# Kernel tuning notes

Measured on AMD Instinct MI355X. Metric: run time of the kernel, lower is better.

The kernel has to match this reference:

```python
import jax, jax.numpy as jnp
import numpy as np

B = 2
D = 256
NH = 8
DH = D // NH
LV = 4
NP_ = 4
NL = 6
DFF = 1024
SHAPES = [(112, 112), (56, 56), (28, 28), (14, 14)]
S = sum(h * w for h, w in SHAPES)


def setup_inputs() -> dict:
    key = jax.random.key(0)
    ks = iter(jax.random.split(key, 64))
    d = {}
    for i, (h, w) in enumerate(SHAPES):
        d[f"src{i}"] = jax.random.normal(next(ks), (B, D, h, w), jnp.float32)
        d[f"pos{i}"] = jax.random.normal(next(ks), (B, D, h, w), jnp.float32)

    def W(*shape, scale=0.02):
        return jax.random.normal(next(ks), shape, jnp.float32) * scale

    d["level_embed"] = W(LV, D, scale=1.0)
    d["off_w"] = W(NL, D, NH * LV * NP_ * 2)
    d["off_b"] = W(NL, NH * LV * NP_ * 2, scale=0.5)
    d["aw_w"] = W(NL, D, NH * LV * NP_)
    d["aw_b"] = jnp.zeros((NL, NH * LV * NP_), jnp.float32)
    d["val_w"] = W(NL, D, D)
    d["val_b"] = jnp.zeros((NL, D), jnp.float32)
    d["out_w"] = W(NL, D, D)
    d["out_b"] = jnp.zeros((NL, D), jnp.float32)
    d["ln1_s"] = jnp.ones((NL, D), jnp.float32)
    d["ln1_b"] = jnp.zeros((NL, D), jnp.float32)
    d["ff1_w"] = W(NL, D, DFF)
    d["ff1_b"] = jnp.zeros((NL, DFF), jnp.float32)
    d["ff2_w"] = W(NL, DFF, D)
    d["ff2_b"] = jnp.zeros((NL, D), jnp.float32)
    d["ln2_s"] = jnp.ones((NL, D), jnp.float32)
    d["ln2_b"] = jnp.zeros((NL, D), jnp.float32)
    return d


def _ln(x, s, b):
    m = jnp.mean(x, -1, keepdims=True)
    v = jnp.mean((x - m) ** 2, -1, keepdims=True)
    return (x - m) / jnp.sqrt(v + 1e-5) * s + b


def _bilinear(v, loc, Hl, Wl):
    # v: [N, DH, Hl, Wl]; loc: [N, Q, P, 2] in [0,1] (grid_sample align_corners=False, zero padding)
    N, Dh = v.shape[0], v.shape[1]
    Q, P = loc.shape[1], loc.shape[2]
    x = loc[..., 0] * Wl - 0.5
    y = loc[..., 1] * Hl - 0.5
    x0f = jnp.floor(x)
    y0f = jnp.floor(y)
    lx = x - x0f
    ly = y - y0f
    x0 = x0f.astype(jnp.int32)
    y0 = y0f.astype(jnp.int32)
    vf = v.reshape(N, Dh, Hl * Wl)

    def g(xi, yi):
        valid = (xi >= 0) & (xi < Wl) & (yi >= 0) & (yi < Hl)
        idx = (jnp.clip(yi, 0, Hl - 1) * Wl + jnp.clip(xi, 0, Wl - 1)).reshape(N, Q * P)
        out = jnp.take_along_axis(vf, idx[:, None, :], axis=2).reshape(N, Dh, Q, P)
        return out * valid[:, None].astype(v.dtype)

    w00 = ((1 - lx) * (1 - ly))[:, None]
    w10 = (lx * (1 - ly))[:, None]
    w01 = ((1 - lx) * ly)[:, None]
    w11 = (lx * ly)[:, None]
    return g(x0, y0) * w00 + g(x0 + 1, y0) * w10 + g(x0, y0 + 1) * w01 + g(x0 + 1, y0 + 1) * w11


def _ms_deform_attn(value, loc, attn):
    # value [B,S,NH,DH], loc [B,S,NH,LV,P,2], attn [B,S,NH,LV,P]
    out = jnp.zeros((B * NH, DH, S), value.dtype)
    s0 = 0
    for l, (Hl, Wl) in enumerate(SHAPES):
        vl = value[:, s0:s0 + Hl * Wl].reshape(B, Hl, Wl, NH, DH)
        vl = vl.transpose(0, 3, 4, 1, 2).reshape(B * NH, DH, Hl, Wl)
        ll = loc[:, :, :, l].transpose(0, 2, 1, 3, 4).reshape(B * NH, S, NP_, 2)
        al = attn[:, :, :, l].transpose(0, 2, 1, 3).reshape(B * NH, S, NP_)[:, None]
        out = out + (_bilinear(vl, ll, Hl, Wl) * al).sum(-1)
        s0 += Hl * Wl
    return out.reshape(B, NH * DH, S).transpose(0, 2, 1)


def _forward(srcs, poss, level_embed, off_w, off_b, aw_w, aw_b, val_w, val_b,
             out_w, out_b, ln1_s, ln1_b, ff1_w, ff1_b, ff2_w, ff2_b, ln2_s, ln2_b):
    src = jnp.concatenate([s.reshape(B, D, -1).transpose(0, 2, 1) for s in srcs], 1)
    pos = jnp.concatenate(
        [p.reshape(B, D, -1).transpose(0, 2, 1) + level_embed[i][None, None] for i, p in enumerate(poss)], 1)
    # reference points: padding masks are all-False => valid_ratios == 1
    refs = []
    for (Hl, Wl) in SHAPES:
        gy, gx = jnp.meshgrid((jnp.arange(Hl) + 0.5) / Hl, (jnp.arange(Wl) + 0.5) / Wl, indexing="ij")
        refs.append(jnp.stack([gx.ravel(), gy.ravel()], -1))
    ref = jnp.concatenate(refs, 0)  # [S, 2]
    normalizer = jnp.array([[w, h] for (h, w) in SHAPES], jnp.float32)  # [LV, 2] = (W, H)
    x = src
    for i in range(NL):
        q = x + pos
        off = (q @ off_w[i] + off_b[i]).reshape(B, S, NH, LV, NP_, 2)
        aw = jax.nn.softmax((q @ aw_w[i] + aw_b[i]).reshape(B, S, NH, LV * NP_), -1)
        aw = aw.reshape(B, S, NH, LV, NP_)
        val = (x @ val_w[i] + val_b[i]).reshape(B, S, NH, DH)
        loc = ref[None, :, None, None, None, :] + off / normalizer[None, None, None, :, None, :]
        attn_out = _ms_deform_attn(val, loc, aw) @ out_w[i] + out_b[i]
        x = _ln(x + attn_out, ln1_s[i], ln1_b[i])
        ff = jax.nn.relu(x @ ff1_w[i] + ff1_b[i]) @ ff2_w[i] + ff2_b[i]
        x = _ln(x + ff, ln2_s[i], ln2_b[i])
    return x


def reference(src0, src1, src2, src3, pos0, pos1, pos2, pos3, level_embed,
              off_w, off_b, aw_w, aw_b, val_w, val_b, out_w, out_b,
              ln1_s, ln1_b, ff1_w, ff1_b, ff2_w, ff2_b, ln2_s, ln2_b):
    memory = _forward([src0, src1, src2, src3], [pos0, pos1, pos2, pos3], level_embed,
                      off_w, off_b, aw_w, aw_b, val_w, val_b, out_w, out_b,
                      ln1_s, ln1_b, ff1_w, ff1_b, ff2_w, ff2_b, ln2_s, ln2_b)
    spatial_shapes = jnp.array(SHAPES, jnp.int32)
    level_start_index = jnp.concatenate(
        [jnp.zeros((1,), jnp.int32), jnp.cumsum(spatial_shapes.prod(1))[:-1].astype(jnp.int32)])
    return memory, spatial_shapes, level_start_index
```

## Files before the change

kernel.cpp:

```cpp
#include <hip/hip_runtime.h>


constexpr int kB  = 2;
constexpr int kD  = 256;
constexpr int kNH = 8;
constexpr int kLV = 4;
constexpr int kNP = 4;
constexpr int kNL = 6;
constexpr int kDFF = 1024;
constexpr int kS  = 16660;
constexpr int kM  = kB * kS;
constexpr int kMp = 33408;
constexpr int kMT64 = kMp / 64;
constexpr int kMT32 = kMp / 32;

typedef short bf16x8 __attribute__((ext_vector_type(8)));
typedef float f32x4  __attribute__((ext_vector_type(4)));

__device__ __forceinline__ unsigned short f2bf(float x) {
  union { float f; unsigned int u; } v; v.f = x;
  unsigned int r = v.u + 0x7FFFu + ((v.u >> 16) & 1u);
  return (unsigned short)(r >> 16);
}
__device__ __forceinline__ float bf2f(unsigned short u) {
  union { unsigned int u; float f; } v; v.u = ((unsigned int)u) << 16;
  return v.f;
}
__device__ __forceinline__ float bflo(unsigned int u) {
  union { unsigned int u; float f; } v; v.u = u << 16;
  return v.f;
}
__device__ __forceinline__ float bfhi(unsigned int u) {
  union { unsigned int u; float f; } v; v.u = u & 0xFFFF0000u;
  return v.f;
}

#define GLOAD_LDS16(gp, lp)                                                    \
  __builtin_amdgcn_global_load_lds(                                            \
      (const __attribute__((address_space(1))) void*)(gp),                     \
      (__attribute__((address_space(3))) void*)(lp), 16, 0, 0)

#define SBARRIER() asm volatile("s_barrier" ::: "memory")

__global__ __launch_bounds__(256) void build_xpos_k(
    const float* __restrict__ src, const float* __restrict__ pos,
    const float* __restrict__ lemb, float* __restrict__ xout,
    float* __restrict__ posout, unsigned short* __restrict__ xbf,
    unsigned short* __restrict__ qbf, int HW, int s0, int lvl)
{
  __shared__ float ts[32][33];
  __shared__ float tp[32][33];
  const int b  = blockIdx.z;
  const int p0 = blockIdx.x * 32, d0 = blockIdx.y * 32;
  const int tx = threadIdx.x, ty = threadIdx.y;
  for (int dd = ty; dd < 32; dd += 8) {
    int p = p0 + tx;
    if (p < HW) {
      size_t idx = ((size_t)b * kD + (d0 + dd)) * (size_t)HW + p;
      ts[dd][tx] = src[idx];
      tp[dd][tx] = pos[idx];
    }
  }
  __syncthreads();
  for (int pp = ty; pp < 32; pp += 8) {
    int p = p0 + pp, d = d0 + tx;
    if (p < HW) {
      size_t o = ((size_t)b * kS + (s0 + p)) * (size_t)kD + d;
      float x = ts[tx][pp];
      float pv = tp[tx][pp] + lemb[lvl * kD + d];
      xout[o] = x;
      posout[o] = pv;
      xbf[o] = f2bf(x);
      qbf[o] = f2bf(x + pv);
    }
  }
}

__global__ __launch_bounds__(256) void wconv_k(
    const float* __restrict__ W, unsigned short* __restrict__ Wt,
    int K, int N, int rowoff, int rowstotal)
{
  __shared__ float t[32][33];
  const int l = blockIdx.z;
  const int n0 = blockIdx.x * 32, k0 = blockIdx.y * 32;
  const int tx = threadIdx.x & 31, ty = threadIdx.x >> 5;
  const float* Wl = W + (size_t)l * K * N;
  unsigned short* Wtl = Wt + (size_t)l * rowstotal * K;
  for (int kk = ty; kk < 32; kk += 8)
    t[kk][tx] = Wl[(size_t)(k0 + kk) * N + n0 + tx];
  __syncthreads();
  for (int nn = ty; nn < 32; nn += 8)
    Wtl[(size_t)(rowoff + n0 + nn) * K + k0 + tx] = f2bf(t[tx][nn]);
}

__global__ __launch_bounds__(256) void biaspack_k(
    const float* __restrict__ ob, const float* __restrict__ ab,
    float* __restrict__ qb)
{
  int i = blockIdx.x * 256 + threadIdx.x;
  if (i >= kNL * 384) return;
  int l = i / 384, c = i - l * 384;
  qb[i] = (c < 256) ? ob[l * 256 + c] : ab[l * 128 + (c - 256)];
}

__global__ __launch_bounds__(256) void refxy_k(float* __restrict__ ref)
{
  int s = blockIdx.x * 256 + threadIdx.x;
  if (s >= kS) return;
  int ls, side;
  if (s < 12544)      { ls = s;         side = 112; }
  else if (s < 15680) { ls = s - 12544; side = 56;  }
  else if (s < 16464) { ls = s - 15680; side = 28;  }
  else                { ls = s - 16464; side = 14;  }
  const float inv = 1.0f / (float)side;
  ref[s * 2 + 0] = ((ls % side) + 0.5f) * inv;
  ref[s * 2 + 1] = ((ls / side) + 0.5f) * inv;
}

template<int RELU, int OUTBF>
__global__ __launch_bounds__(256) void hgemm64_k(
    const unsigned short* __restrict__ A, const unsigned short* __restrict__ Bt,
    const float* __restrict__ bias, void* __restrict__ Cout, int N, int K)
{
  __shared__ unsigned short As[2][64 * 32];
  __shared__ unsigned short Bs[2][128 * 32];
  const int tid = threadIdx.x;
  const int bm = blockIdx.y * 64;
  const int bn = blockIdx.x * 128;
  const int lane = tid & 63;
  const int wave = tid >> 6;
  const int wr = (wave >> 1) * 32, wc = (wave & 1) * 64;
  const int l15 = lane & 15, l4 = lane >> 4;

  f32x4 acc[2][4] = {};

  const unsigned short* A0 = A + (size_t)(bm + (tid >> 2)) * K + ((tid & 3) << 3);
  const int cb1 = 256 + tid;
  const unsigned short* B0 = Bt + (size_t)(bn + (tid >> 2)) * K + ((tid & 3) << 3);
  const unsigned short* B1 = Bt + (size_t)(bn + (cb1 >> 2)) * K + ((cb1 & 3) << 3);

#define STAGE64(buf, k0)                                                       \
  do {                                                                         \
    GLOAD_LDS16(A0 + (k0), (char*)As[buf] + tid * 16);                         \
    GLOAD_LDS16(B0 + (k0), (char*)Bs[buf] + tid * 16);                         \
    GLOAD_LDS16(B1 + (k0), (char*)Bs[buf] + cb1 * 16);                         \
  } while (0)

  const int nt = K >> 5;
  STAGE64(0, 0);
  STAGE64(1, 32);
  for (int k = 0; k < nt; ++k) {
    if (k + 1 < nt) asm volatile("s_waitcnt vmcnt(3)" ::: "memory");
    else            asm volatile("s_waitcnt vmcnt(0)" ::: "memory");
    SBARRIER();
    __builtin_amdgcn_sched_barrier(0);
    const int cur = k & 1;
    bf16x8 af[2], bfr[4];
#pragma unroll
    for (int m = 0; m < 2; ++m)
      af[m] = *(const bf16x8*)&As[cur][(wr + m * 16 + l15) * 32 + l4 * 8];
#pragma unroll
    for (int n = 0; n < 4; ++n)
      bfr[n] = *(const bf16x8*)&Bs[cur][(wc + n * 16 + l15) * 32 + l4 * 8];
#pragma unroll
    for (int m = 0; m < 2; ++m)
#pragma unroll
      for (int n = 0; n < 4; ++n)
        acc[m][n] = __builtin_amdgcn_mfma_f32_16x16x32_bf16(
            af[m], bfr[n], acc[m][n], 0, 0, 0);
    SBARRIER();
    if (k + 2 < nt) STAGE64(cur, (k + 2) * 32);
  }
#undef STAGE64

#pragma unroll
  for (int n = 0; n < 4; ++n) {
    const int col = bn + wc + n * 16 + l15;
    const float bv = bias[col];
#pragma unroll
    for (int m = 0; m < 2; ++m) {
#pragma unroll
      for (int j = 0; j < 4; ++j) {
        const int row = bm + wr + m * 16 + l4 * 4 + j;
        float v = acc[m][n][j] + bv;
        if (RELU) v = fmaxf(v, 0.f);
        if (OUTBF)
          ((unsigned short*)Cout)[(size_t)row * N + col] = f2bf(v);
        else
          ((float*)Cout)[(size_t)row * N + col] = v;
      }
    }
  }
}

__global__ __launch_bounds__(256) void qvgemm_k(
    const unsigned short* __restrict__ Aq, const unsigned short* __restrict__ Ax,
    const unsigned short* __restrict__ Bq, const unsigned short* __restrict__ Bv,
    const float* __restrict__ biasq, const float* __restrict__ biasv,
    float* __restrict__ Cq, unsigned short* __restrict__ Cv)
{
  constexpr int K = 256;
  __shared__ unsigned short As[2][64 * 32];
  __shared__ unsigned short Bs[2][128 * 32];
  const int tid = threadIdx.x;
  const int bx = blockIdx.x;
  const bool isv = bx >= 3;
  const int bn = (isv ? bx - 3 : bx) * 128;
  const int bm = blockIdx.y * 64;
  const unsigned short* A  = isv ? Ax : Aq;
  const unsigned short* Bt = isv ? Bv : Bq;
  const float* bias = isv ? biasv : biasq;
  const int lane = tid & 63;
  const int wave = tid >> 6;
  const int wr = (wave >> 1) * 32, wc = (wave & 1) * 64;
  const int l15 = lane & 15, l4 = lane >> 4;

  f32x4 acc[2][4] = {};

  const unsigned short* A0 = A + (size_t)(bm + (tid >> 2)) * K + ((tid & 3) << 3);
  const int cb1 = 256 + tid;
  const unsigned short* B0 = Bt + (size_t)(bn + (tid >> 2)) * K + ((tid & 3) << 3);
  const unsigned short* B1 = Bt + (size_t)(bn + (cb1 >> 2)) * K + ((cb1 & 3) << 3);

#define STAGEQV(buf, k0)                                                       \
  do {                                                                         \
    GLOAD_LDS16(A0 + (k0), (char*)As[buf] + tid * 16);                         \
    GLOAD_LDS16(B0 + (k0), (char*)Bs[buf] + tid * 16);                         \
    GLOAD_LDS16(B1 + (k0), (char*)Bs[buf] + cb1 * 16);                         \
  } while (0)

  const int nt = K >> 5;
  STAGEQV(0, 0);
  STAGEQV(1, 32);
  for (int k = 0; k < nt; ++k) {
    if (k + 1 < nt) asm volatile("s_waitcnt vmcnt(3)" ::: "memory");
    else            asm volatile("s_waitcnt vmcnt(0)" ::: "memory");
    SBARRIER();
    __builtin_amdgcn_sched_barrier(0);
    const int cur = k & 1;
    bf16x8 af[2], bfr[4];
#pragma unroll
    for (int m = 0; m < 2; ++m)
      af[m] = *(const bf16x8*)&As[cur][(wr + m * 16 + l15) * 32 + l4 * 8];
#pragma unroll
    for (int n = 0; n < 4; ++n)
      bfr[n] = *(const bf16x8*)&Bs[cur][(wc + n * 16 + l15) * 32 + l4 * 8];
#pragma unroll
    for (int m = 0; m < 2; ++m)
#pragma unroll
      for (int n = 0; n < 4; ++n)
        acc[m][n] = __builtin_amdgcn_mfma_f32_16x16x32_bf16(
            af[m], bfr[n], acc[m][n], 0, 0, 0);
    SBARRIER();
    if (k + 2 < nt) STAGEQV(cur, (k + 2) * 32);
  }
#undef STAGEQV

#pragma unroll
  for (int n = 0; n < 4; ++n) {
    const int col = bn + wc + n * 16 + l15;
    const float bv = bias[col];
#pragma unroll
    for (int m = 0; m < 2; ++m) {
#pragma unroll
      for (int j = 0; j < 4; ++j) {
        const int row = bm + wr + m * 16 + l4 * 4 + j;
        float v = acc[m][n][j] + bv;
        if (isv)
          Cv[(size_t)row * 256 + col] = f2bf(v);
        else
          Cq[(size_t)row * 384 + col] = v;
      }
    }
  }
}

template<int WQ, int OUTDST>
__global__ __launch_bounds__(256) void hgemmln_k(
    const unsigned short* __restrict__ A, const unsigned short* __restrict__ Bt,
    const float* __restrict__ bias, const float* __restrict__ Rsd,
    const float* __restrict__ g, const float* __restrict__ beta,
    const float* __restrict__ posb, float* __restrict__ yout,
    unsigned short* __restrict__ xbf, unsigned short* __restrict__ qbf, int K)
{
  __shared__ unsigned short As[2][32 * 32];
  __shared__ unsigned short Bs[2][256 * 32];
  __shared__ float ssum[32][5];
  __shared__ float ssq[32][5];
  const int tid = threadIdx.x;
  const int bm = blockIdx.x * 32;
  const int lane = tid & 63;
  const int wave = tid >> 6;
  const int wc = wave * 64;
  const int l15 = lane & 15, l4 = lane >> 4;

  f32x4 acc[2][4] = {};

  const unsigned short* Aq = A + (size_t)(bm + (tid >> 2)) * K + ((tid & 3) << 3);
  const unsigned short* Bq0 = Bt + (size_t)(0 * 64 + (tid >> 2)) * K + ((tid & 3) << 3);
  const unsigned short* Bq1 = Bt + (size_t)(1 * 64 + (tid >> 2)) * K + ((tid & 3) << 3);
  const unsigned short* Bq2 = Bt + (size_t)(2 * 64 + (tid >> 2)) * K + ((tid & 3) << 3);
  const unsigned short* Bq3 = Bt + (size_t)(3 * 64 + (tid >> 2)) * K + ((tid & 3) << 3);

#define STAGE_LN(buf, k0)                                                      \
  do {                                                                         \
    if (tid < 128) GLOAD_LDS16(Aq + (k0), (char*)As[buf] + tid * 16);          \
    GLOAD_LDS16(Bq0 + (k0), (char*)Bs[buf] + (0 * 256 + tid) * 16);            \
    GLOAD_LDS16(Bq1 + (k0), (char*)Bs[buf] + (1 * 256 + tid) * 16);            \
    GLOAD_LDS16(Bq2 + (k0), (char*)Bs[buf] + (2 * 256 + tid) * 16);            \
    GLOAD_LDS16(Bq3 + (k0), (char*)Bs[buf] + (3 * 256 + tid) * 16);            \
  } while (0)

  const int nt = K >> 5;
  STAGE_LN(0, 0);
  STAGE_LN(1, 32);
  for (int k = 0; k < nt; ++k) {
    if (k + 1 < nt) {
      if (wave < 2) asm volatile("s_waitcnt vmcnt(5)" ::: "memory");
      else          asm volatile("s_waitcnt vmcnt(4)" ::: "memory");
    } else {
      asm volatile("s_waitcnt vmcnt(0)" ::: "memory");
    }
    SBARRIER();
    __builtin_amdgcn_sched_barrier(0);
    const int cur = k & 1;
    bf16x8 af[2], bfr[4];
#pragma unroll
    for (int m = 0; m < 2; ++m)
      af[m] = *(const bf16x8*)&As[cur][(m * 16 + l15) * 32 + l4 * 8];
#pragma unroll
    for (int n = 0; n < 4; ++n)
      bfr[n] = *(const bf16x8*)&Bs[cur][(wc + n * 16 + l15) * 32 + l4 * 8];
#pragma unroll
    for (int m = 0; m < 2; ++m)
#pragma unroll
      for (int n = 0; n < 4; ++n)
        acc[m][n] = __builtin_amdgcn_mfma_f32_16x16x32_bf16(
            af[m], bfr[n], acc[m][n], 0, 0, 0);
    SBARRIER();
    if (k + 2 < nt) STAGE_LN(cur, (k + 2) * 32);
  }
#undef STAGE_LN

  float bv[4], gv[4], btv[4];
#pragma unroll
  for (int n = 0; n < 4; ++n) {
    const int col = wc + n * 16 + l15;
    bv[n] = bias[col];
    gv[n] = g[col];
    btv[n] = beta[col];
  }
#pragma unroll
  for (int m = 0; m < 2; ++m) {
#pragma unroll
    for (int j = 0; j < 4; ++j) {
      const int row = bm + m * 16 + l4 * 4 + j;
#pragma unroll
      for (int n = 0; n < 4; ++n)
        acc[m][n][j] += bv[n] + Rsd[(size_t)row * kD + wc + n * 16 + l15];
    }
  }
#pragma unroll
  for (int m = 0; m < 2; ++m) {
#pragma unroll
    for (int j = 0; j < 4; ++j) {
      float s = acc[m][0][j] + acc[m][1][j] + acc[m][2][j] + acc[m][3][j];
      float q = acc[m][0][j] * acc[m][0][j] + acc[m][1][j] * acc[m][1][j] +
                acc[m][2][j] * acc[m][2][j] + acc[m][3][j] * acc[m][3][j];
#pragma unroll
      for (int d2 = 1; d2 < 16; d2 <<= 1) {
        s += __shfl_xor(s, d2, 64);
        q += __shfl_xor(q, d2, 64);
      }
      if (l15 == 0) {
        const int r = m * 16 + l4 * 4 + j;
        ssum[r][wave] = s;
        ssq[r][wave] = q;
      }
    }
  }
  __syncthreads();
#pragma unroll
  for (int m = 0; m < 2; ++m) {
#pragma unroll
    for (int j = 0; j < 4; ++j) {
      const int r = m * 16 + l4 * 4 + j;
      const int row = bm + r;
      const float mean = (ssum[r][0] + ssum[r][1] + ssum[r][2] + ssum[r][3]) *
                         (1.0f / kD);
      const float var = (ssq[r][0] + ssq[r][1] + ssq[r][2] + ssq[r][3]) *
                        (1.0f / kD) - mean * mean;
      const float rstd = rsqrtf(var + 1e-5f);
      if (row < kM) {
#pragma unroll
        for (int n = 0; n < 4; ++n) {
          const int col = wc + n * 16 + l15;
          const float y = (acc[m][n][j] - mean) * rstd * gv[n] + btv[n];
          const size_t o = (size_t)row * kD + col;
          if (OUTDST) {
            yout[o] = y;
          } else {
            yout[o] = y;
            xbf[o] = f2bf(y);
            if (WQ) qbf[o] = f2bf(y + posb[o]);
          }
        }
      }
    }
  }
}

__global__ __launch_bounds__(256) void msdeform_k(
    const unsigned short* __restrict__ val, const float* __restrict__ qout,
    const float* __restrict__ ref, unsigned short* __restrict__ outbf)
{
  __shared__ int   sIdx[4][8][128];
  __shared__ float sW[4][8][128];
  const int bs0 = blockIdx.x * 8;
  const int tid = threadIdx.x;

#pragma unroll
  for (int it = 0; it < 4; ++it) {
    const int item = tid + it * 256;
    const int q = item >> 7;
    const int t = item & 127;
    const int bs = bs0 + q;
    const int b = bs / kS, s = bs - b * kS;
    const int l = (t & 15) >> 2;

    const float logit = qout[(size_t)bs * 384 + 256 + t];
    float mx = logit;
#pragma unroll
    for (int d2 = 1; d2 < 16; d2 <<= 1) mx = fmaxf(mx, __shfl_xor(mx, d2, 64));
    float e = __expf(logit - mx);
    float sm = e;
#pragma unroll
    for (int d2 = 1; d2 < 16; d2 <<= 1) sm += __shfl_xor(sm, d2, 64);
    const float a = e / sm;

    const float rfx = ref[s * 2 + 0];
    const float rfy = ref[s * 2 + 1];
    const int side  = 112 >> l;
    const int start = (l >= 1 ? 12544 : 0) + (l >= 2 ? 3136 : 0) + (l >= 3 ? 784 : 0);
    const float ox = qout[(size_t)bs * 384 + t * 2 + 0];
    const float oy = qout[(size_t)bs * 384 + t * 2 + 1];
    const float xx = fmaf(rfx, (float)side, ox) - 0.5f;
    const float yy = fmaf(rfy, (float)side, oy) - 0.5f;
    const float xf = floorf(xx), yf = floorf(yy);
    const float lx = xx - xf, ly = yy - yf;
    const int x0 = (int)xf, y0 = (int)yf;
    const float w00 = (1.f - lx) * (1.f - ly) * a, w10 = lx * (1.f - ly) * a;
    const float w01 = (1.f - lx) * ly * a,         w11 = lx * ly * a;
    const bool xv0 = (unsigned)x0 < (unsigned)side, xv1 = (unsigned)(x0 + 1) < (unsigned)side;
    const bool yv0 = (unsigned)y0 < (unsigned)side, yv1 = (unsigned)(y0 + 1) < (unsigned)side;
    const int cx0 = min(max(x0, 0), side - 1), cx1 = min(max(x0 + 1, 0), side - 1);
    const int cy0 = min(max(y0, 0), side - 1), cy1 = min(max(y0 + 1, 0), side - 1);
    const int rowbase = b * kS + start;
    const int t2 = (t & 15) * 8 + (t >> 4);
    sIdx[0][q][t2] = (rowbase + cy0 * side + cx0) << 9;
    sIdx[1][q][t2] = (rowbase + cy0 * side + cx1) << 9;
    sIdx[2][q][t2] = (rowbase + cy1 * side + cx0) << 9;
    sIdx[3][q][t2] = (rowbase + cy1 * side + cx1) << 9;
    sW[0][q][t2] = (xv0 && yv0) ? w00 : 0.f;
    sW[1][q][t2] = (xv1 && yv0) ? w10 : 0.f;
    sW[2][q][t2] = (xv0 && yv1) ? w01 : 0.f;
    sW[3][q][t2] = (xv1 && yv1) ? w11 : 0.f;
  }
  __syncthreads();

  const int q  = tid >> 5;
  const int h  = (tid >> 2) & 7;
  const int l4 = tid & 3;
  const char* vbase = (const char*)val + h * 64 + l4 * 16;

  float a0 = 0.f, a1 = 0.f, a2 = 0.f, a3 = 0.f;
  float a4 = 0.f, a5 = 0.f, a6 = 0.f, a7 = 0.f;
#pragma unroll
  for (int sp = 0; sp < 16; ++sp) {
    const int t2 = sp * 8 + h;
#pragma unroll
    for (int c = 0; c < 4; ++c) {
      const int off = sIdx[c][q][t2];
      const float w = sW[c][q][t2];
      const uint4 v = *(const uint4*)(vbase + off);
      a0 = fmaf(w, bflo(v.x), a0); a1 = fmaf(w, bfhi(v.x), a1);
      a2 = fmaf(w, bflo(v.y), a2); a3 = fmaf(w, bfhi(v.y), a3);
      a4 = fmaf(w, bflo(v.z), a4); a5 = fmaf(w, bfhi(v.z), a5);
      a6 = fmaf(w, bflo(v.w), a6); a7 = fmaf(w, bfhi(v.w), a7);
    }
  }
  bf16x8 o;
  o[0] = (short)f2bf(a0); o[1] = (short)f2bf(a1);
  o[2] = (short)f2bf(a2); o[3] = (short)f2bf(a3);
  o[4] = (short)f2bf(a4); o[5] = (short)f2bf(a5);
  o[6] = (short)f2bf(a6); o[7] = (short)f2bf(a7);
  *(bf16x8*)(outbf + (size_t)(bs0 + q) * 256 + h * 32 + l4 * 8) = o;
}

__global__ void tail_k(float* __restrict__ out)
{
  if (threadIdx.x == 0) {
    const size_t n = (size_t)kM * kD;
    out[n + 0] = 112.f; out[n + 1] = 112.f;
    out[n + 2] = 56.f;  out[n + 3] = 56.f;
    out[n + 4] = 28.f;  out[n + 5] = 28.f;
    out[n + 6] = 14.f;  out[n + 7] = 14.f;
    out[n + 8] = 0.f;   out[n + 9] = 12544.f;
    out[n + 10] = 15680.f; out[n + 11] = 16464.f;
  }
}

extern "C" void kernel_launch(void* const* d_in, const int* in_sizes, int n_in,
                              void* d_out, int out_size, void* d_ws, size_t ws_size,
                              hipStream_t stream)
{
  const float* src[4] = {(const float*)d_in[0], (const float*)d_in[2],
                         (const float*)d_in[4], (const float*)d_in[6]};
  const float* pos[4] = {(const float*)d_in[1], (const float*)d_in[3],
                         (const float*)d_in[5], (const float*)d_in[7]};
  const float* lemb  = (const float*)d_in[8];
  const float* off_w = (const float*)d_in[9];
  const float* off_b = (const float*)d_in[10];
  const float* aw_w  = (const float*)d_in[11];
  const float* aw_b  = (const float*)d_in[12];
  const float* val_w = (const float*)d_in[13];
  const float* val_b = (const float*)d_in[14];
  const float* out_w = (const float*)d_in[15];
  const float* out_b = (const float*)d_in[16];
  const float* ln1_s = (const float*)d_in[17];
  const float* ln1_b = (const float*)d_in[18];
  const float* ff1_w = (const float*)d_in[19];
  const float* ff1_b = (const float*)d_in[20];
  const float* ff2_w = (const float*)d_in[21];
  const float* ff2_b = (const float*)d_in[22];
  const float* ln2_s = (const float*)d_in[23];
  const float* ln2_b = (const float*)d_in[24];

  const size_t SZ = (size_t)kMp * kD;
  float* ws   = (float*)d_ws;
  float* posb = (float*)d_out;
  float* xb   = ws;
  float* R    = ws + SZ;
  float* qout = R;
  unsigned short* valbf = (unsigned short*)(R + SZ + SZ / 2);
  unsigned short* attbf = (unsigned short*)(R + 2 * SZ);
  unsigned short* ffbf  = (unsigned short*)R;
  unsigned short* qbf   = (unsigned short*)(ws + 3 * SZ);
  unsigned short* xbf   = qbf + SZ;
  unsigned short* wts   = (unsigned short*)(ws + 4 * SZ);
  unsigned short* qwT  = wts;
  unsigned short* valT = qwT + kNL * 384 * 256;
  unsigned short* outT = valT + kNL * 256 * 256;
  unsigned short* ff1T = outT + kNL * 256 * 256;
  unsigned short* ff2T = ff1T + kNL * 1024 * 256;
  float* qbias = (float*)(ff2T + kNL * 256 * 1024);
  float* reftab = qbias + kNL * 384;

  wconv_k<<<dim3(256 / 32, 256 / 32, kNL), 256, 0, stream>>>(off_w, qwT, 256, 256, 0, 384);
  wconv_k<<<dim3(128 / 32, 256 / 32, kNL), 256, 0, stream>>>(aw_w,  qwT, 256, 128, 256, 384);
  wconv_k<<<dim3(256 / 32, 256 / 32, kNL), 256, 0, stream>>>(val_w, valT, 256, 256, 0, 256);
  wconv_k<<<dim3(256 / 32, 256 / 32, kNL), 256, 0, stream>>>(out_w, outT, 256, 256, 0, 256);
  wconv_k<<<dim3(1024 / 32, 256 / 32, kNL), 256, 0, stream>>>(ff1_w, ff1T, 256, 1024, 0, 1024);
  wconv_k<<<dim3(256 / 32, 1024 / 32, kNL), 256, 0, stream>>>(ff2_w, ff2T, 1024, 256, 0, 256);
  biaspack_k<<<(kNL * 384 + 255) / 256, 256, 0, stream>>>(off_b, aw_b, qbias);
  refxy_k<<<(kS + 255) / 256, 256, 0, stream>>>(reftab);

  const int sides[4]  = {112, 56, 28, 14};
  const int starts[4] = {0, 12544, 15680, 16464};
  for (int l = 0; l < 4; ++l) {
    int HW = sides[l] * sides[l];
    dim3 g((HW + 31) / 32, kD / 32, kB);
    build_xpos_k<<<g, dim3(32, 8), 0, stream>>>(src[l], pos[l], lemb, xb, posb,
                                                xbf, qbf, HW, starts[l], l);
  }

  const dim3 blk(256);
  for (int i = 0; i < kNL; ++i) {
    qvgemm_k<<<dim3(5, kMT64), blk, 0, stream>>>(
        qbf, xbf, qwT + (size_t)i * 384 * 256, valT + (size_t)i * 256 * 256,
        qbias + i * 384, val_b + i * 256, qout, valbf);
    msdeform_k<<<kM / 8, blk, 0, stream>>>(valbf, qout, reftab, attbf);
    hgemmln_k<0, 0><<<kMT32, blk, 0, stream>>>(
        attbf, outT + (size_t)i * 256 * 256, out_b + i * 256, xb,
        ln1_s + i * kD, ln1_b + i * kD, nullptr, xb, xbf, nullptr, 256);
    hgemm64_k<1, 1><<<dim3(8, kMT64), blk, 0, stream>>>(
        xbf, ff1T + (size_t)i * 1024 * 256, ff1_b + i * 1024, ffbf, 1024, 256);
    if (i < kNL - 1) {
      hgemmln_k<1, 0><<<kMT32, blk, 0, stream>>>(
          ffbf, ff2T + (size_t)i * 256 * 1024, ff2_b + i * 256, xb,
          ln2_s + i * kD, ln2_b + i * kD, posb, xb, xbf, qbf, 1024);
    } else {
      hgemmln_k<0, 1><<<kMT32, blk, 0, stream>>>(
          ffbf, ff2T + (size_t)i * 256 * 1024, ff2_b + i * 256, xb,
          ln2_s + i * kD, ln2_b + i * kD, nullptr, (float*)d_out, nullptr,
          nullptr, 1024);
    }
  }

  tail_k<<<1, 64, 0, stream>>>((float*)d_out);
}
```

Baseline: 1.425 ms.

## Store pos and query projections in 16-bit, triple-buffer A tiles, remap deform blocks per XCD

```diff
diff --git a/kernel.cpp b/kernel.cpp
--- a/kernel.cpp
+++ b/kernel.cpp
@@ -45,7 +45,7 @@
 __global__ __launch_bounds__(256) void build_xpos_k(
     const float* __restrict__ src, const float* __restrict__ pos,
     const float* __restrict__ lemb, float* __restrict__ xout,
-    float* __restrict__ posout, unsigned short* __restrict__ xbf,
+    unsigned short* __restrict__ posbf, unsigned short* __restrict__ xbf,
     unsigned short* __restrict__ qbf, int HW, int s0, int lvl)
 {
   __shared__ float ts[32][33];
@@ -69,7 +69,7 @@
       float x = ts[tx][pp];
       float pv = tp[tx][pp] + lemb[lvl * kD + d];
       xout[o] = x;
-      posout[o] = pv;
+      posbf[o] = f2bf(pv);
       xbf[o] = f2bf(x);
       qbf[o] = f2bf(x + pv);
     }
@@ -197,7 +197,7 @@
     const unsigned short* __restrict__ Aq, const unsigned short* __restrict__ Ax,
     const unsigned short* __restrict__ Bq, const unsigned short* __restrict__ Bv,
     const float* __restrict__ biasq, const float* __restrict__ biasv,
-    float* __restrict__ Cq, unsigned short* __restrict__ Cv)
+    _Float16* __restrict__ Cq, unsigned short* __restrict__ Cv)
 {
   constexpr int K = 256;
   __shared__ unsigned short As[2][64 * 32];
@@ -269,7 +269,7 @@
         if (isv)
           Cv[(size_t)row * 256 + col] = f2bf(v);
         else
-          Cq[(size_t)row * 384 + col] = v;
+          Cq[(size_t)row * 384 + col] = (_Float16)v;
       }
     }
   }
@@ -280,13 +280,13 @@
     const unsigned short* __restrict__ A, const unsigned short* __restrict__ Bt,
     const float* __restrict__ bias, const float* __restrict__ Rsd,
     const float* __restrict__ g, const float* __restrict__ beta,
-    const float* __restrict__ posb, float* __restrict__ yout,
+    const unsigned short* __restrict__ posbf, float* __restrict__ yout,
     unsigned short* __restrict__ xbf, unsigned short* __restrict__ qbf, int K)
 {
-  __shared__ unsigned short As[2][32 * 32];
+  __shared__ unsigned short As[3][32 * 32];
   __shared__ unsigned short Bs[2][256 * 32];
-  __shared__ float ssum[32][5];
-  __shared__ float ssq[32][5];
+  float* ssum = (float*)&As[0][0];
+  float* ssq  = ssum + 32 * 5;
   const int tid = threadIdx.x;
   const int bm = blockIdx.x * 32;
   const int lane = tid & 63;
@@ -302,9 +302,12 @@
   const unsigned short* Bq2 = Bt + (size_t)(2 * 64 + (tid >> 2)) * K + ((tid & 3) << 3);
   const unsigned short* Bq3 = Bt + (size_t)(3 * 64 + (tid >> 2)) * K + ((tid & 3) << 3);
 
-#define STAGE_LN(buf, k0)                                                      \
+#define STA(buf, k0)                                                           \
   do {                                                                         \
     if (tid < 128) GLOAD_LDS16(Aq + (k0), (char*)As[buf] + tid * 16);          \
+  } while (0)
+#define STB(buf, k0)                                                           \
+  do {                                                                         \
     GLOAD_LDS16(Bq0 + (k0), (char*)Bs[buf] + (0 * 256 + tid) * 16);            \
     GLOAD_LDS16(Bq1 + (k0), (char*)Bs[buf] + (1 * 256 + tid) * 16);            \
     GLOAD_LDS16(Bq2 + (k0), (char*)Bs[buf] + (2 * 256 + tid) * 16);            \
@@ -312,25 +315,32 @@
   } while (0)
 
   const int nt = K >> 5;
-  STAGE_LN(0, 0);
-  STAGE_LN(1, 32);
+  STB(0, 0);
+  STB(1, 32);
+  STA(0, 0);
+  STA(1, 32);
+  STA(2, 64);
+  int ab = 0;
   for (int k = 0; k < nt; ++k) {
-    if (k + 1 < nt) {
-      if (wave < 2) asm volatile("s_waitcnt vmcnt(5)" ::: "memory");
+    if (k == 0) {
+      if (wave < 2) asm volatile("s_waitcnt vmcnt(2)" ::: "memory");
+      else          asm volatile("s_waitcnt vmcnt(4)" ::: "memory");
+    } else if (k < nt - 3) {
+      if (wave < 2) asm volatile("s_waitcnt vmcnt(6)" ::: "memory");
       else          asm volatile("s_waitcnt vmcnt(4)" ::: "memory");
     } else {
       asm volatile("s_waitcnt vmcnt(0)" ::: "memory");
     }
     SBARRIER();
     __builtin_amdgcn_sched_barrier(0);
-    const int cur = k & 1;
+    const int bcur = k & 1;
     bf16x8 af[2], bfr[4];
 #pragma unroll
     for (int m = 0; m < 2; ++m)
-      af[m] = *(const bf16x8*)&As[cur][(m * 16 + l15) * 32 + l4 * 8];
+      af[m] = *(const bf16x8*)&As[ab][(m * 16 + l15) * 32 + l4 * 8];
 #pragma unroll
     for (int n = 0; n < 4; ++n)
-      bfr[n] = *(const bf16x8*)&Bs[cur][(wc + n * 16 + l15) * 32 + l4 * 8];
+      bfr[n] = *(const bf16x8*)&Bs[bcur][(wc + n * 16 + l15) * 32 + l4 * 8];
 #pragma unroll
     for (int m = 0; m < 2; ++m)
 #pragma unroll
@@ -338,9 +348,12 @@
         acc[m][n] = __builtin_amdgcn_mfma_f32_16x16x32_bf16(
             af[m], bfr[n], acc[m][n], 0, 0, 0);
     SBARRIER();
-    if (k + 2 < nt) STAGE_LN(cur, (k + 2) * 32);
-  }
-#undef STAGE_LN
+    if (k + 2 < nt) STB(bcur, (k + 2) * 32);
+    if (k + 3 < nt) STA(ab, (k + 3) * 32);
+    ab = (ab == 2) ? 0 : ab + 1;
+  }
+#undef STA
+#undef STB
 
   float bv[4], gv[4], btv[4];
 #pragma unroll
@@ -374,8 +387,8 @@
       }
       if (l15 == 0) {
         const int r = m * 16 + l4 * 4 + j;
-        ssum[r][wave] = s;
-        ssq[r][wave] = q;
+        ssum[r * 5 + wave] = s;
+        ssq[r * 5 + wave] = q;
       }
     }
   }
@@ -386,10 +399,10 @@
     for (int j = 0; j < 4; ++j) {
       const int r = m * 16 + l4 * 4 + j;
       const int row = bm + r;
-      const float mean = (ssum[r][0] + ssum[r][1] + ssum[r][2] + ssum[r][3]) *
-                         (1.0f / kD);
-      const float var = (ssq[r][0] + ssq[r][1] + ssq[r][2] + ssq[r][3]) *
-                        (1.0f / kD) - mean * mean;
+      const float mean = (ssum[r * 5 + 0] + ssum[r * 5 + 1] + ssum[r * 5 + 2] +
+                          ssum[r * 5 + 3]) * (1.0f / kD);
+      const float var = (ssq[r * 5 + 0] + ssq[r * 5 + 1] + ssq[r * 5 + 2] +
+                         ssq[r * 5 + 3]) * (1.0f / kD) - mean * mean;
       const float rstd = rsqrtf(var + 1e-5f);
       if (row < kM) {
 #pragma unroll
@@ -402,7 +415,7 @@
           } else {
             yout[o] = y;
             xbf[o] = f2bf(y);
-            if (WQ) qbf[o] = f2bf(y + posb[o]);
+            if (WQ) qbf[o] = f2bf(y + bf2f(posbf[o]));
           }
         }
       }
@@ -411,12 +424,16 @@
 }
 
 __global__ __launch_bounds__(256) void msdeform_k(
-    const unsigned short* __restrict__ val, const float* __restrict__ qout,
+    const unsigned short* __restrict__ val, const _Float16* __restrict__ qout,
     const float* __restrict__ ref, unsigned short* __restrict__ outbf)
 {
   __shared__ int   sIdx[4][8][128];
   __shared__ float sW[4][8][128];
-  const int bs0 = blockIdx.x * 8;
+  const int bid = blockIdx.x;
+  const int xcd = bid & 7;
+  const int jj  = bid >> 3;
+  const int wg  = (xcd < 5 ? xcd * 521 : 5 * 521 + (xcd - 5) * 520) + jj;
+  const int bs0 = wg * 8;
   const int tid = threadIdx.x;
 
 #pragma unroll
@@ -428,7 +445,7 @@
     const int b = bs / kS, s = bs - b * kS;
     const int l = (t & 15) >> 2;
 
-    const float logit = qout[(size_t)bs * 384 + 256 + t];
+    const float logit = (float)qout[(size_t)bs * 384 + 256 + t];
     float mx = logit;
 #pragma unroll
     for (int d2 = 1; d2 < 16; d2 <<= 1) mx = fmaxf(mx, __shfl_xor(mx, d2, 64));
@@ -442,8 +459,8 @@
     const float rfy = ref[s * 2 + 1];
     const int side  = 112 >> l;
     const int start = (l >= 1 ? 12544 : 0) + (l >= 2 ? 3136 : 0) + (l >= 3 ? 784 : 0);
-    const float ox = qout[(size_t)bs * 384 + t * 2 + 0];
-    const float oy = qout[(size_t)bs * 384 + t * 2 + 1];
+    const float ox = (float)qout[(size_t)bs * 384 + t * 2 + 0];
+    const float oy = (float)qout[(size_t)bs * 384 + t * 2 + 1];
     const float xx = fmaf(rfx, (float)side, ox) - 0.5f;
     const float yy = fmaf(rfy, (float)side, oy) - 0.5f;
     const float xf = floorf(xx), yf = floorf(yy);
@@ -538,16 +555,15 @@
 
   const size_t SZ = (size_t)kMp * kD;
   float* ws   = (float*)d_ws;
-  float* posb = (float*)d_out;
   float* xb   = ws;
-  float* R    = ws + SZ;
-  float* qout = R;
-  unsigned short* valbf = (unsigned short*)(R + SZ + SZ / 2);
-  unsigned short* attbf = (unsigned short*)(R + 2 * SZ);
-  unsigned short* ffbf  = (unsigned short*)R;
-  unsigned short* qbf   = (unsigned short*)(ws + 3 * SZ);
+  _Float16* qoutH = (_Float16*)(ws + SZ);
+  unsigned short* valbf = (unsigned short*)(ws + SZ + (3 * SZ) / 4);
+  unsigned short* attbf = valbf + SZ;
+  unsigned short* ffbf  = (unsigned short*)(ws + SZ);
+  unsigned short* posbf = (unsigned short*)(ws + 3 * SZ);
+  unsigned short* qbf   = posbf + SZ;
   unsigned short* xbf   = qbf + SZ;
-  unsigned short* wts   = (unsigned short*)(ws + 4 * SZ);
+  unsigned short* wts   = (unsigned short*)(ws + 4 * SZ + SZ / 2);
   unsigned short* qwT  = wts;
   unsigned short* valT = qwT + kNL * 384 * 256;
   unsigned short* outT = valT + kNL * 256 * 256;
@@ -570,7 +586,7 @@
   for (int l = 0; l < 4; ++l) {
     int HW = sides[l] * sides[l];
     dim3 g((HW + 31) / 32, kD / 32, kB);
-    build_xpos_k<<<g, dim3(32, 8), 0, stream>>>(src[l], pos[l], lemb, xb, posb,
+    build_xpos_k<<<g, dim3(32, 8), 0, stream>>>(src[l], pos[l], lemb, xb, posbf,
                                                 xbf, qbf, HW, starts[l], l);
   }
 
@@ -578,8 +594,8 @@
   for (int i = 0; i < kNL; ++i) {
     qvgemm_k<<<dim3(5, kMT64), blk, 0, stream>>>(
         qbf, xbf, qwT + (size_t)i * 384 * 256, valT + (size_t)i * 256 * 256,
-        qbias + i * 384, val_b + i * 256, qout, valbf);
-    msdeform_k<<<kM / 8, blk, 0, stream>>>(valbf, qout, reftab, attbf);
+        qbias + i * 384, val_b + i * 256, qoutH, valbf);
+    msdeform_k<<<kM / 8, blk, 0, stream>>>(valbf, qoutH, reftab, attbf);
     hgemmln_k<0, 0><<<kMT32, blk, 0, stream>>>(
         attbf, outT + (size_t)i * 256 * 256, out_b + i * 256, xb,
         ln1_s + i * kD, ln1_b + i * kD, nullptr, xb, xbf, nullptr, 256);
@@ -588,7 +604,7 @@
     if (i < kNL - 1) {
       hgemmln_k<1, 0><<<kMT32, blk, 0, stream>>>(
           ffbf, ff2T + (size_t)i * 256 * 1024, ff2_b + i * 256, xb,
-          ln2_s + i * kD, ln2_b + i * kD, posb, xb, xbf, qbf, 1024);
+          ln2_s + i * kD, ln2_b + i * kD, posbf, xb, xbf, qbf, 1024);
     } else {
       hgemmln_k<0, 1><<<kMT32, blk, 0, stream>>>(
           ffbf, ff2T + (size_t)i * 256 * 1024, ff2_b + i * 256, xb,
```

Measured after the change: 1.381 ms. 3.1% less time.
